# Performance work log

Hardware: AMD Instinct MI355X
Metric: run time of the kernel (lower is better)

The kernel has to match this reference:

```python
import jax, jax.numpy as jnp
import numpy as np
from jax import lax
from jax.scipy.special import logsumexp

B, T, H, K = 64, 512, 1024, 8


def crf_nll(logits, tags, mask, trans):
    """Negative log-likelihood summed over batch (allennlp-style linear-chain CRF,
    no start/end transitions). logits [B,T,K], tags [B,T] int, mask [B,T] float, trans [K,K]."""
    def step(alpha, x):
        logit_t, m_t = x  # [B,K], [B]
        inner = alpha[:, :, None] + trans[None, :, :] + logit_t[:, None, :]  # [B,K,K]
        new = logsumexp(inner, axis=1)
        alpha = jnp.where(m_t[:, None] > 0, new, alpha)
        return alpha, None
    alpha, _ = lax.scan(step, logits[:, 0], (jnp.swapaxes(logits[:, 1:], 0, 1), mask[:, 1:].T))
    logZ = logsumexp(alpha, axis=-1)  # [B]
    emit = jnp.take_along_axis(logits, tags[..., None], axis=-1)[..., 0]  # [B,T]
    emit_score = jnp.sum(emit * mask, axis=-1)
    trans_score = jnp.sum(trans[tags[:, :-1], tags[:, 1:]] * mask[:, 1:], axis=-1)
    return -jnp.sum(emit_score + trans_score - logZ)


def viterbi(logits, trans):
    """Batched Viterbi decode with all-ones mask (as in the original forward).
    logits [B,T,K], trans [K,K] -> tags [B,T] int."""
    def step(alpha, logit_t):
        scores = alpha[:, :, None] + trans[None, :, :]  # [B,K_prev,K_next]
        bp = jnp.argmax(scores, axis=1)                 # [B,K]
        alpha = jnp.max(scores, axis=1) + logit_t
        return alpha, bp
    alpha, bps = lax.scan(step, logits[:, 0], jnp.swapaxes(logits[:, 1:], 0, 1))
    last = jnp.argmax(alpha, axis=-1)  # [B]
    def back(tag, bp):
        prev = jnp.take_along_axis(bp, tag[:, None], axis=1)[:, 0]
        return prev, prev
    _, prevs = lax.scan(back, last, bps, reverse=True)  # [T-1,B]
    return jnp.concatenate([prevs, last[None, :]], axis=0).T  # [B,T]


def setup_inputs():
    key = jax.random.key(0)
    ks = jax.random.split(key, 12)
    encoding = jax.random.normal(ks[0], (B, T, H), dtype=jnp.float32)
    raw = jax.random.randint(ks[1], (B, 3 * T), 0, K).astype(jnp.int32)
    offsets = jnp.concatenate([jnp.zeros(T, jnp.int32), jnp.full((T,), 8, jnp.int32), jnp.full((T,), 16, jnp.int32)])
    labels = raw + offsets[None, :]
    len_tokens = jax.random.randint(ks[2], (B,), 1, T + 1).astype(jnp.int32)
    s = 1.0 / np.sqrt(H)
    W_task = jax.random.uniform(ks[3], (H, K), jnp.float32, -s, s)
    b_task = jax.random.uniform(ks[4], (K,), jnp.float32, -s, s)
    W_process = jax.random.uniform(ks[5], (H, K), jnp.float32, -s, s)
    b_process = jax.random.uniform(ks[6], (K,), jnp.float32, -s, s)
    W_material = jax.random.uniform(ks[7], (H, K), jnp.float32, -s, s)
    b_material = jax.random.uniform(ks[8], (K,), jnp.float32, -s, s)
    trans_task = jax.random.normal(ks[9], (K, K), jnp.float32) * 0.1
    trans_process = jax.random.normal(ks[10], (K, K), jnp.float32) * 0.1
    trans_material = jax.random.normal(ks[11], (K, K), jnp.float32) * 0.1
    return {"encoding": encoding, "labels": labels, "len_tokens": len_tokens,
            "W_task": W_task, "b_task": b_task, "W_process": W_process, "b_process": b_process,
            "W_material": W_material, "b_material": b_material,
            "trans_task": trans_task, "trans_process": trans_process, "trans_material": trans_material}


def reference(encoding, labels, len_tokens, W_task, b_task, W_process, b_process,
              W_material, b_material, trans_task, trans_process, trans_material):
    task_logits = encoding @ W_task + b_task          # [B,T,K]
    process_logits = encoding @ W_process + b_process
    material_logits = encoding @ W_material + b_material
    logits3 = jnp.stack([task_logits, process_logits, material_logits])   # [3,B,T,K]
    trans3 = jnp.stack([trans_task, trans_process, trans_material])       # [3,K,K]
    # Viterbi with all-ones mask, as in the original forward
    tags3 = jax.vmap(viterbi)(logits3, trans3)  # [3,B,T]
    predicted_tags = jnp.concatenate([tags3[0], tags3[1] + 8, tags3[2] + 16], axis=1)  # [B,3T]
    # CRF NLL losses with length mask (training/validation path)
    mask = (jnp.arange(T)[None, :] < len_tokens[:, None]).astype(jnp.float32)
    labels3 = jnp.stack([labels[:, :T], labels[:, T:2 * T] - 8, labels[:, 2 * T:] - 16])
    loss = jnp.sum(jax.vmap(crf_nll, in_axes=(0, 0, None, 0))(logits3, labels3, mask, trans3))
    return task_logits, process_logits, material_logits, predicted_tags, loss
```

## Files before the change

kernel.cpp:

```cpp
#include <hip/hip_runtime.h>
#include <hip/hip_bf16.h>
#include <math.h>

#define BATCH 64
#define TT 512
#define HH 1024
#define KK 8
#define ROWS (BATCH * TT)
#define SEG  (ROWS * KK)
#define TAGS_OFF (3 * SEG)
#define LOSS_OFF (TAGS_OFF + BATCH * 3 * TT)

__global__ __launch_bounds__(256, 2) void gemm_heads(
    const float* __restrict__ enc,
    const float* __restrict__ Wt, const float* __restrict__ bt,
    const float* __restrict__ Wp, const float* __restrict__ bpv,
    const float* __restrict__ Wm, const float* __restrict__ bm,
    float* __restrict__ out)
{
    __shared__ float xt[4][2][16][68];
    __shared__ float wl[4][2][16][32];
    __shared__ float biasl[24];

    int tid  = threadIdx.x;
    int lane = tid & 63;
    int w    = __builtin_amdgcn_readfirstlane(tid >> 6);
    int r    = lane >> 2;
    int q    = lane & 3;
    int rowblk = blockIdx.x * 64;

    if (tid < 24) {
        int hd = tid >> 3, cl = tid & 7;
        biasl[tid] = (hd == 0) ? bt[cl] : (hd == 1) ? bpv[cl] : bm[cl];
    }

    const float* encw = enc + (size_t)rowblk * HH + w * 256;
    const float* Wkt = Wt + w * 2048;
    const float* Wkp = Wp + w * 2048;
    const float* Wkm = Wm + w * 2048;

    int srow = lane >> 2;
    int schunk = lane & 3;

    float acc[24];
#pragma unroll
    for (int c = 0; c < 24; ++c) acc[c] = 0.f;

    float4 sreg[4];
    float  wreg[6];

#define LOADT(it)                                                             \
    {                                                                         \
        _Pragma("unroll")                                                     \
        for (int i = 0; i < 4; ++i)                                           \
            sreg[i] = *(const float4*)(encw + (size_t)(srow + 16 * i) * HH +  \
                                       (it) * 16 + schunk * 4);               \
    }
#define WRITET(buf)                                                           \
    {                                                                         \
        _Pragma("unroll")                                                     \
        for (int i = 0; i < 4; ++i) {                                         \
            xt[w][buf][schunk * 4 + 0][srow + 16 * i] = sreg[i].x;            \
            xt[w][buf][schunk * 4 + 1][srow + 16 * i] = sreg[i].y;            \
            xt[w][buf][schunk * 4 + 2][srow + 16 * i] = sreg[i].z;            \
            xt[w][buf][schunk * 4 + 3][srow + 16 * i] = sreg[i].w;            \
        }                                                                     \
    }
#define WLOADG(it)                                                            \
    {                                                                         \
        wreg[0] = Wkt[(it) * 128 + lane]; wreg[1] = Wkt[(it) * 128 + 64 + lane]; \
        wreg[2] = Wkp[(it) * 128 + lane]; wreg[3] = Wkp[(it) * 128 + 64 + lane]; \
        wreg[4] = Wkm[(it) * 128 + lane]; wreg[5] = Wkm[(it) * 128 + 64 + lane]; \
    }
#define WWRITE(buf)                                                           \
    {                                                                         \
        int col_ = lane & 7;                                                  \
        _Pragma("unroll")                                                     \
        for (int i = 0; i < 6; ++i) {                                         \
            int hh_ = (lane >> 3) + 8 * (i & 1);                              \
            int c_  = 8 * (i >> 1) + col_;                                    \
            int q_  = (c_ * 43) >> 8;                                         \
            int s_  = c_ - 6 * q_;                                            \
            wl[w][buf][hh_][8 * (q_ ^ (hh_ & 3)) + s_] = wreg[i];             \
        }                                                                     \
    }

    LOADT(0)
    WLOADG(0)
    WRITET(0)
    WWRITE(0)

    for (int it = 0; it < 16; ++it) {
        int cb = it & 1;
        if (it < 15) {
            LOADT(it + 1)
            WLOADG(it + 1)
        }
#pragma unroll
        for (int hh = 0; hh < 16; ++hh) {
            float4 xv = *(const float4*)&xt[w][cb][hh][4 * r];
            const float* wp_ = &wl[w][cb][hh][8 * (q ^ (hh & 3))];
            float4 w0 = *(const float4*)wp_;
            float2 w1 = *(const float2*)(wp_ + 4);
#pragma unroll
            for (int j = 0; j < 4; ++j) {
                float xe = (j == 0) ? xv.x : (j == 1) ? xv.y : (j == 2) ? xv.z : xv.w;
                acc[j * 6 + 0] = fmaf(xe, w0.x, acc[j * 6 + 0]);
                acc[j * 6 + 1] = fmaf(xe, w0.y, acc[j * 6 + 1]);
                acc[j * 6 + 2] = fmaf(xe, w0.z, acc[j * 6 + 2]);
                acc[j * 6 + 3] = fmaf(xe, w0.w, acc[j * 6 + 3]);
                acc[j * 6 + 4] = fmaf(xe, w1.x, acc[j * 6 + 4]);
                acc[j * 6 + 5] = fmaf(xe, w1.y, acc[j * 6 + 5]);
            }
        }
        if (it < 15) {
            WRITET(cb ^ 1)
            WWRITE(cb ^ 1)
        }
    }
#undef LOADT
#undef WRITET
#undef WLOADG
#undef WWRITE

    __syncthreads();
    float* xf = &xt[0][0][0][0];
    int myrow = 4 * r;
    if (w != 0) {
        float* sl = xf + w * 1600;
#pragma unroll
        for (int j = 0; j < 4; ++j)
#pragma unroll
            for (int s = 0; s < 6; ++s)
                sl[(myrow + j) * 25 + q * 6 + s] = acc[j * 6 + s];
    }
    __syncthreads();
    if (w == 0) {
#pragma unroll
        for (int j = 0; j < 4; ++j)
#pragma unroll
            for (int s = 0; s < 6; ++s)
                xf[(myrow + j) * 25 + q * 6 + s] =
                    acc[j * 6 + s] + xf[1600 + (myrow + j) * 25 + q * 6 + s]
                                   + xf[3200 + (myrow + j) * 25 + q * 6 + s]
                                   + xf[4800 + (myrow + j) * 25 + q * 6 + s];
    }
    __syncthreads();
#pragma unroll
    for (int i = 0; i < 2; ++i) {
        int flat = tid + 256 * i;
        if (flat < 384) {
            int seg  = flat >> 7;
            int rem  = flat & 127;
            int row  = rem >> 1;
            int half = rem & 1;
            float4 v;
            v.x = xf[row * 25 + seg * 8 + half * 4 + 0] + biasl[seg * 8 + half * 4 + 0];
            v.y = xf[row * 25 + seg * 8 + half * 4 + 1] + biasl[seg * 8 + half * 4 + 1];
            v.z = xf[row * 25 + seg * 8 + half * 4 + 2] + biasl[seg * 8 + half * 4 + 2];
            v.w = xf[row * 25 + seg * 8 + half * 4 + 3] + biasl[seg * 8 + half * 4 + 3];
            *(float4*)(out + (size_t)seg * SEG + (size_t)(rowblk + row) * 8 + half * 4) = v;
        }
    }
}

#define DPPF(x, ctrl) __int_as_float(__builtin_amdgcn_update_dpp(              \
    0, __float_as_int(x), ctrl, 0xF, 0xF, true))

__device__ __forceinline__ float bcast8(float x, int lane) {
    float qv = DPPF(x, 0x00);
    float hv = DPPF(qv, 0x141);
    return (lane & 4) ? hv : qv;
}

#define GATHER8(ao, r0, r1, r2, r3, r4, r5, r6, r7)                            \
    {                                                                          \
        float s1_ = DPPF(ao, 0xB1);                                            \
        float s2_ = DPPF(ao, 0x4E);                                            \
        float s3_ = DPPF(s1_, 0x4E);                                           \
        float s7_ = DPPF(ao, 0x141);                                           \
        float s6_ = DPPF(s1_, 0x141);                                          \
        float s5_ = DPPF(s2_, 0x141);                                          \
        float s4_ = DPPF(s3_, 0x141);                                          \
        r0 = ao; r1 = s1_; r2 = s2_; r3 = s3_;                                 \
        r4 = s7_; r5 = s6_; r6 = s5_; r7 = s4_;                                \
    }

__device__ __forceinline__ float rfl(float x) {
    return __int_as_float(__builtin_amdgcn_readfirstlane(__float_as_int(x)));
}

__global__ __launch_bounds__(128) void crf_vit(
    const float* __restrict__ logits,
    const int* __restrict__ labels,
    const int* __restrict__ lens,
    const float* __restrict__ trans_t,
    const float* __restrict__ trans_p,
    const float* __restrict__ trans_m,
    float* __restrict__ out_tags,
    float* __restrict__ partial)
{
    __shared__ float llds[TT * KK];
    __shared__ __align__(16) float alds[TT * KK];
    __shared__ unsigned bpw[TT * 2];
    __shared__ unsigned fmapw[64][2];
    __shared__ unsigned char bnd[64];

    int blk = blockIdx.x;
    int h   = blk >> 6;
    int b   = blk & 63;
    int tid = threadIdx.x;
    int wid = __builtin_amdgcn_readfirstlane(tid >> 6);
    int lane = tid & 63;
    int p = lane & 7;
    unsigned char* bpb = (unsigned char*)bpw;

    const float* L = logits + ((size_t)h * BATCH + b) * (TT * KK);
    const float4* Lv = (const float4*)L;
    float4* lv = (float4*)llds;
#pragma unroll
    for (int i = 0; i < 8; ++i) lv[tid + 128 * i] = Lv[tid + 128 * i];
    __syncthreads();

    const float* TR = (h == 0) ? trans_t : (h == 1) ? trans_p : trans_m;
    int len = lens[b];

    if (wid == 0) {
        float Tc0 = TR[(p ^ 0) * 8 + p], Tc1 = TR[(p ^ 1) * 8 + p];
        float Tc2 = TR[(p ^ 2) * 8 + p], Tc3 = TR[(p ^ 3) * 8 + p];
        float Tc4 = TR[(p ^ 7) * 8 + p], Tc5 = TR[(p ^ 6) * 8 + p];
        float Tc6 = TR[(p ^ 5) * 8 + p], Tc7 = TR[(p ^ 4) * 8 + p];

        float av = llds[p];
        if (lane < 8) alds[lane] = av;
        float r0, r1, r2, r3, r4, r5, r6, r7;
        GATHER8(av, r0, r1, r2, r3, r4, r5, r6, r7)

#define VSTEP(t, LT)                                                           \
    {                                                                          \
        float m0 = r0 + Tc0, m1 = r1 + Tc1, m2 = r2 + Tc2, m3 = r3 + Tc3;      \
        float m4 = r4 + Tc4, m5 = r5 + Tc5, m6 = r6 + Tc6, m7 = r7 + Tc7;      \
        float x01 = fmaxf(m0, m1), x23 = fmaxf(m2, m3);                        \
        float x45 = fmaxf(m4, m5), x67 = fmaxf(m6, m7);                        \
        av = fmaxf(fmaxf(x01, x23), fmaxf(x45, x67)) + (LT);                   \
        if (lane < 8) alds[(t) * 8 + p] = av;                                  \
        GATHER8(av, r0, r1, r2, r3, r4, r5, r6, r7)                            \
    }

        for (int c = 0; c < 15; ++c) {
            int tb = 1 + 32 * c;
            float lt[32];
#pragma unroll
            for (int j = 0; j < 32; ++j) lt[j] = llds[(tb + j) * 8 + p];
            __builtin_amdgcn_sched_barrier(0);
#pragma unroll
            for (int j = 0; j < 32; ++j) VSTEP(tb + j, lt[j])
        }
        {
            float lt[31];
#pragma unroll
            for (int j = 0; j < 31; ++j) lt[j] = llds[(481 + j) * 8 + p];
            __builtin_amdgcn_sched_barrier(0);
#pragma unroll
            for (int j = 0; j < 31; ++j) VSTEP(481 + j, lt[j])
        }
#undef VSTEP

        asm volatile("" ::: "memory");

        float4 f03 = *(const float4*)&alds[511 * 8];
        float4 f47 = *(const float4*)&alds[511 * 8 + 4];
        float fv = f03.x; int last_ = 0; float nf;
        nf = f03.y; if (nf > fv) { fv = nf; last_ = 1; }
        nf = f03.z; if (nf > fv) { fv = nf; last_ = 2; }
        nf = f03.w; if (nf > fv) { fv = nf; last_ = 3; }
        nf = f47.x; if (nf > fv) { fv = nf; last_ = 4; }
        nf = f47.y; if (nf > fv) { fv = nf; last_ = 5; }
        nf = f47.z; if (nf > fv) { fv = nf; last_ = 6; }
        nf = f47.w; if (nf > fv) { fv = nf; last_ = 7; }

        {
            int c = lane >> 3;
            int kn = lane & 7;
            float T0 = TR[0 * 8 + kn], T1 = TR[1 * 8 + kn];
            float T2 = TR[2 * 8 + kn], T3 = TR[3 * 8 + kn];
            float T4 = TR[4 * 8 + kn], T5 = TR[5 * 8 + kn];
            float T6 = TR[6 * 8 + kn], T7 = TR[7 * 8 + kn];
            for (int j = 0; j < 64; ++j) {
                int t = c * 64 + j + 1;
                if (t <= 511) {
                    float4 a03 = *(const float4*)&alds[(t - 1) * 8];
                    float4 a47 = *(const float4*)&alds[(t - 1) * 8 + 4];
                    float v = a03.x + T0; int vi = 0; float nv;
                    nv = a03.y + T1; if (nv > v) { v = nv; vi = 1; }
                    nv = a03.z + T2; if (nv > v) { v = nv; vi = 2; }
                    nv = a03.w + T3; if (nv > v) { v = nv; vi = 3; }
                    nv = a47.x + T4; if (nv > v) { v = nv; vi = 4; }
                    nv = a47.y + T5; if (nv > v) { v = nv; vi = 5; }
                    nv = a47.z + T6; if (nv > v) { v = nv; vi = 6; }
                    nv = a47.w + T7; if (nv > v) { v = nv; vi = 7; }
                    bpb[t * 8 + kn] = (unsigned char)vi;
                }
            }
        }
        asm volatile("" ::: "memory");

        int t0 = lane * 8;
        unsigned rw[16];
#pragma unroll
        for (int j = 0; j < 8; ++j) {
            int t = t0 + 1 + j;
            if (t <= 511) { rw[2 * j] = bpw[t * 2]; rw[2 * j + 1] = bpw[t * 2 + 1]; }
            else          { rw[2 * j] = 0x03020100u; rw[2 * j + 1] = 0x07060504u; }
        }
        unsigned sv[8];
#pragma unroll
        for (int i = 0; i < 8; ++i) sv[i] = i;
#pragma unroll
        for (int j = 7; j >= 0; --j) {
            unsigned d0 = rw[2 * j], d1 = rw[2 * j + 1];
#pragma unroll
            for (int i = 0; i < 8; ++i) {
                unsigned s = sv[i];
                unsigned d = (s < 4) ? d0 : d1;
                sv[i] = (d >> (8 * (s & 3))) & 0xffu;
            }
        }
        fmapw[lane][0] = sv[0] | (sv[1] << 8) | (sv[2] << 16) | (sv[3] << 24);
        fmapw[lane][1] = sv[4] | (sv[5] << 8) | (sv[6] << 16) | (sv[7] << 24);
        asm volatile("" ::: "memory");

        if (lane == 0) {
            unsigned cur = (unsigned)last_;
            for (int l = 63; l >= 0; --l) {
                unsigned d = (cur < 4) ? fmapw[l][0] : fmapw[l][1];
                cur = (d >> (8 * (cur & 3))) & 0xffu;
                bnd[l] = (unsigned char)cur;
            }
        }
        asm volatile("" ::: "memory");

        int off = h * 8;
        float* otag = out_tags + b * (3 * TT) + h * TT;
        unsigned curr = (lane == 63) ? (unsigned)last_ : (unsigned)bnd[lane + 1];
#pragma unroll
        for (int j = 7; j >= 0; --j) {
            unsigned d = (curr < 4) ? rw[2 * j] : rw[2 * j + 1];
            curr = (d >> (8 * (curr & 3))) & 0xffu;
            otag[t0 + j] = (float)((int)curr + off);
        }
    } else {
        float E0 = __expf(TR[(p ^ 0) * 8 + p]), E1 = __expf(TR[(p ^ 1) * 8 + p]);
        float E2 = __expf(TR[(p ^ 2) * 8 + p]), E3 = __expf(TR[(p ^ 3) * 8 + p]);
        float E4 = __expf(TR[(p ^ 7) * 8 + p]), E5 = __expf(TR[(p ^ 6) * 8 + p]);
        float E6 = __expf(TR[(p ^ 5) * 8 + p]), E7 = __expf(TR[(p ^ 4) * 8 + p]);

        float a0 = llds[p];
        float c0 = bcast8(a0, lane);
        float S  = __expf(a0 - c0);
        float Mc = c0;

#define LSTEP(t, F_, RN)                                                       \
    {                                                                          \
        if (RN) {                                                              \
            float sref = bcast8(S, lane);                                      \
            float gg = __logf(sref);                                           \
            S *= __expf(-gg);                                                  \
            Mc += gg;                                                          \
        }                                                                      \
        float r0, r1, r2, r3, r4, r5, r6, r7;                                  \
        GATHER8(S, r0, r1, r2, r3, r4, r5, r6, r7)                             \
        float p0 = r0 * E0, p1 = r1 * E1, p2 = r2 * E2, p3 = r3 * E3;          \
        float p4 = r4 * E4, p5 = r5 * E5, p6 = r6 * E6, p7 = r7 * E7;          \
        float ss = ((p0 + p1) + (p2 + p3)) + ((p4 + p5) + (p6 + p7));          \
        float Sn = ss * (F_);                                                  \
        S = ((t) < len) ? Sn : S;                                              \
    }

        for (int c = 0; c < 15; ++c) {
            int tb = 1 + 32 * c;
            float F[32];
#pragma unroll
            for (int j = 0; j < 32; ++j) F[j] = llds[(tb + j) * 8 + p];
#pragma unroll
            for (int j = 0; j < 32; ++j) F[j] = __expf(F[j]);
            __builtin_amdgcn_sched_barrier(0);
#pragma unroll
            for (int j = 0; j < 32; ++j) LSTEP(tb + j, F[j], (j & 3) == 0)
        }
        {
            float F[31];
#pragma unroll
            for (int j = 0; j < 31; ++j) F[j] = llds[(481 + j) * 8 + p];
#pragma unroll
            for (int j = 0; j < 31; ++j) F[j] = __expf(F[j]);
            __builtin_amdgcn_sched_barrier(0);
#pragma unroll
            for (int j = 0; j < 31; ++j) LSTEP(481 + j, F[j], (j & 3) == 0)
        }
#undef LSTEP

        float s1 = S + DPPF(S, 0xB1);
        float s2 = s1 + DPPF(s1, 0x4E);
        float sum8 = s2 + DPPF(s2, 0x141);
        float logZ = Mc + __logf(sum8);

        const int* lab = labels + b * (3 * TT) + h * TT;
        int off = h * 8;
        float sc = 0.f;
#pragma unroll
        for (int j = 0; j < 8; ++j) {
            int t = lane + 64 * j;
            if (t < len) {
                int tg = lab[t] - off;
                sc += llds[t * 8 + tg];
                if (t >= 1) {
                    int tp = lab[t - 1] - off;
                    sc += TR[tp * 8 + tg];
                }
            }
        }
#pragma unroll
        for (int d = 1; d <= 32; d <<= 1) sc += __shfl_xor(sc, d);

        if (lane == 0) partial[blk] = logZ - sc;
    }
}

__global__ __launch_bounds__(64) void loss_reduce(
    const float* __restrict__ partial, float* __restrict__ out_loss)
{
    int lane = threadIdx.x;
    float s = partial[lane] + partial[lane + 64] + partial[lane + 128];
#pragma unroll
    for (int d = 1; d <= 32; d <<= 1) s += __shfl_xor(s, d);
    if (lane == 0) *out_loss = s;
}

extern "C" void kernel_launch(void* const* d_in, const int* in_sizes, int n_in,
                              void* d_out, int out_size, void* d_ws, size_t ws_size,
                              hipStream_t stream) {
    const float* enc    = (const float*)d_in[0];
    const int*   labels = (const int*)d_in[1];
    const int*   lens   = (const int*)d_in[2];
    const float* Wt     = (const float*)d_in[3];
    const float* bt     = (const float*)d_in[4];
    const float* Wp     = (const float*)d_in[5];
    const float* bpv    = (const float*)d_in[6];
    const float* Wm     = (const float*)d_in[7];
    const float* bm     = (const float*)d_in[8];
    const float* tr_t   = (const float*)d_in[9];
    const float* tr_p   = (const float*)d_in[10];
    const float* tr_m   = (const float*)d_in[11];

    float* out = (float*)d_out;
    float* lpart = (float*)d_ws;

    gemm_heads<<<ROWS / 64, 256, 0, stream>>>(enc, Wt, bt, Wp, bpv, Wm, bm, out);
    crf_vit<<<192, 128, 0, stream>>>(out, labels, lens, tr_t, tr_p, tr_m,
                                     out + TAGS_OFF, lpart);
    loss_reduce<<<1, 64, 0, stream>>>(lpart, out + LOSS_OFF);
}
```

Before: 70.55 us.

## Merge Viterbi and forward-algorithm waves into one interleaved single-wave CRF kernel

The CRF kernel previously used two waves per block, one computing the Viterbi max recurrence and backtrace and the other the logsumexp partition function. Both recurrences now run in a single 64-thread wave, interleaved per time step so each dependency chain can hide the other's latency. The forward-algorithm renormalization is restructured so its log/exp is applied one group later, off the critical chain. This trades wave-level concurrency for instruction-level parallelism and halves the block size, and it serializes the backtrace and the label score after both recursions.

```diff
diff --git a/kernel.cpp b/kernel.cpp
--- a/kernel.cpp
+++ b/kernel.cpp
@@ -186,11 +186,7 @@
         r4 = s7_; r5 = s6_; r6 = s5_; r7 = s4_;                                \
     }
 
-__device__ __forceinline__ float rfl(float x) {
-    return __int_as_float(__builtin_amdgcn_readfirstlane(__float_as_int(x)));
-}
-
-__global__ __launch_bounds__(128) void crf_vit(
+__global__ __launch_bounds__(64) void crf_vit(
     const float* __restrict__ logits,
     const int* __restrict__ labels,
     const int* __restrict__ lens,
@@ -209,9 +205,7 @@
     int blk = blockIdx.x;
     int h   = blk >> 6;
     int b   = blk & 63;
-    int tid = threadIdx.x;
-    int wid = __builtin_amdgcn_readfirstlane(tid >> 6);
-    int lane = tid & 63;
+    int lane = threadIdx.x;
     int p = lane & 7;
     unsigned char* bpb = (unsigned char*)bpw;
 
@@ -219,154 +213,44 @@
     const float4* Lv = (const float4*)L;
     float4* lv = (float4*)llds;
 #pragma unroll
-    for (int i = 0; i < 8; ++i) lv[tid + 128 * i] = Lv[tid + 128 * i];
+    for (int i = 0; i < 16; ++i) lv[lane + 64 * i] = Lv[lane + 64 * i];
     __syncthreads();
 
     const float* TR = (h == 0) ? trans_t : (h == 1) ? trans_p : trans_m;
     int len = lens[b];
 
-    if (wid == 0) {
-        float Tc0 = TR[(p ^ 0) * 8 + p], Tc1 = TR[(p ^ 1) * 8 + p];
-        float Tc2 = TR[(p ^ 2) * 8 + p], Tc3 = TR[(p ^ 3) * 8 + p];
-        float Tc4 = TR[(p ^ 7) * 8 + p], Tc5 = TR[(p ^ 6) * 8 + p];
-        float Tc6 = TR[(p ^ 5) * 8 + p], Tc7 = TR[(p ^ 4) * 8 + p];
-
-        float av = llds[p];
-        if (lane < 8) alds[lane] = av;
-        float r0, r1, r2, r3, r4, r5, r6, r7;
-        GATHER8(av, r0, r1, r2, r3, r4, r5, r6, r7)
-
-#define VSTEP(t, LT)                                                           \
+    float Tc0 = TR[(p ^ 0) * 8 + p], Tc1 = TR[(p ^ 1) * 8 + p];
+    float Tc2 = TR[(p ^ 2) * 8 + p], Tc3 = TR[(p ^ 3) * 8 + p];
+    float Tc4 = TR[(p ^ 7) * 8 + p], Tc5 = TR[(p ^ 6) * 8 + p];
+    float Tc6 = TR[(p ^ 5) * 8 + p], Tc7 = TR[(p ^ 4) * 8 + p];
+    float E0 = __expf(Tc0), E1 = __expf(Tc1), E2 = __expf(Tc2), E3 = __expf(Tc3);
+    float E4 = __expf(Tc4), E5 = __expf(Tc5), E6 = __expf(Tc6), E7 = __expf(Tc7);
+
+    float av = llds[p];
+    if (lane < 8) alds[lane] = av;
+    float c0 = bcast8(av, lane);
+    float S  = __expf(av - c0);
+    float Mc = c0;
+    float g = 0.f, eg = 1.f;
+
+#define VSTEP(LT, AVH)                                                         \
     {                                                                          \
+        float r0, r1, r2, r3, r4, r5, r6, r7;                                  \
+        GATHER8(av, r0, r1, r2, r3, r4, r5, r6, r7)                            \
         float m0 = r0 + Tc0, m1 = r1 + Tc1, m2 = r2 + Tc2, m3 = r3 + Tc3;      \
         float m4 = r4 + Tc4, m5 = r5 + Tc5, m6 = r6 + Tc6, m7 = r7 + Tc7;      \
         float x01 = fmaxf(m0, m1), x23 = fmaxf(m2, m3);                        \
         float x45 = fmaxf(m4, m5), x67 = fmaxf(m6, m7);                        \
         av = fmaxf(fmaxf(x01, x23), fmaxf(x45, x67)) + (LT);                   \
-        if (lane < 8) alds[(t) * 8 + p] = av;                                  \
-        GATHER8(av, r0, r1, r2, r3, r4, r5, r6, r7)                            \
-    }
-
-        for (int c = 0; c < 15; ++c) {
-            int tb = 1 + 32 * c;
-            float lt[32];
-#pragma unroll
-            for (int j = 0; j < 32; ++j) lt[j] = llds[(tb + j) * 8 + p];
-            __builtin_amdgcn_sched_barrier(0);
-#pragma unroll
-            for (int j = 0; j < 32; ++j) VSTEP(tb + j, lt[j])
-        }
-        {
-            float lt[31];
-#pragma unroll
-            for (int j = 0; j < 31; ++j) lt[j] = llds[(481 + j) * 8 + p];
-            __builtin_amdgcn_sched_barrier(0);
-#pragma unroll
-            for (int j = 0; j < 31; ++j) VSTEP(481 + j, lt[j])
-        }
-#undef VSTEP
-
-        asm volatile("" ::: "memory");
-
-        float4 f03 = *(const float4*)&alds[511 * 8];
-        float4 f47 = *(const float4*)&alds[511 * 8 + 4];
-        float fv = f03.x; int last_ = 0; float nf;
-        nf = f03.y; if (nf > fv) { fv = nf; last_ = 1; }
-        nf = f03.z; if (nf > fv) { fv = nf; last_ = 2; }
-        nf = f03.w; if (nf > fv) { fv = nf; last_ = 3; }
-        nf = f47.x; if (nf > fv) { fv = nf; last_ = 4; }
-        nf = f47.y; if (nf > fv) { fv = nf; last_ = 5; }
-        nf = f47.z; if (nf > fv) { fv = nf; last_ = 6; }
-        nf = f47.w; if (nf > fv) { fv = nf; last_ = 7; }
-
-        {
-            int c = lane >> 3;
-            int kn = lane & 7;
-            float T0 = TR[0 * 8 + kn], T1 = TR[1 * 8 + kn];
-            float T2 = TR[2 * 8 + kn], T3 = TR[3 * 8 + kn];
-            float T4 = TR[4 * 8 + kn], T5 = TR[5 * 8 + kn];
-            float T6 = TR[6 * 8 + kn], T7 = TR[7 * 8 + kn];
-            for (int j = 0; j < 64; ++j) {
-                int t = c * 64 + j + 1;
-                if (t <= 511) {
-                    float4 a03 = *(const float4*)&alds[(t - 1) * 8];
-                    float4 a47 = *(const float4*)&alds[(t - 1) * 8 + 4];
-                    float v = a03.x + T0; int vi = 0; float nv;
-                    nv = a03.y + T1; if (nv > v) { v = nv; vi = 1; }
-                    nv = a03.z + T2; if (nv > v) { v = nv; vi = 2; }
-                    nv = a03.w + T3; if (nv > v) { v = nv; vi = 3; }
-                    nv = a47.x + T4; if (nv > v) { v = nv; vi = 4; }
-                    nv = a47.y + T5; if (nv > v) { v = nv; vi = 5; }
-                    nv = a47.z + T6; if (nv > v) { v = nv; vi = 6; }
-                    nv = a47.w + T7; if (nv > v) { v = nv; vi = 7; }
-                    bpb[t * 8 + kn] = (unsigned char)vi;
-                }
-            }
-        }
-        asm volatile("" ::: "memory");
-
-        int t0 = lane * 8;
-        unsigned rw[16];
-#pragma unroll
-        for (int j = 0; j < 8; ++j) {
-            int t = t0 + 1 + j;
-            if (t <= 511) { rw[2 * j] = bpw[t * 2]; rw[2 * j + 1] = bpw[t * 2 + 1]; }
-            else          { rw[2 * j] = 0x03020100u; rw[2 * j + 1] = 0x07060504u; }
-        }
-        unsigned sv[8];
-#pragma unroll
-        for (int i = 0; i < 8; ++i) sv[i] = i;
-#pragma unroll
-        for (int j = 7; j >= 0; --j) {
-            unsigned d0 = rw[2 * j], d1 = rw[2 * j + 1];
-#pragma unroll
-            for (int i = 0; i < 8; ++i) {
-                unsigned s = sv[i];
-                unsigned d = (s < 4) ? d0 : d1;
-                sv[i] = (d >> (8 * (s & 3))) & 0xffu;
-            }
-        }
-        fmapw[lane][0] = sv[0] | (sv[1] << 8) | (sv[2] << 16) | (sv[3] << 24);
-        fmapw[lane][1] = sv[4] | (sv[5] << 8) | (sv[6] << 16) | (sv[7] << 24);
-        asm volatile("" ::: "memory");
-
-        if (lane == 0) {
-            unsigned cur = (unsigned)last_;
-            for (int l = 63; l >= 0; --l) {
-                unsigned d = (cur < 4) ? fmapw[l][0] : fmapw[l][1];
-                cur = (d >> (8 * (cur & 3))) & 0xffu;
-                bnd[l] = (unsigned char)cur;
-            }
-        }
-        asm volatile("" ::: "memory");
-
-        int off = h * 8;
-        float* otag = out_tags + b * (3 * TT) + h * TT;
-        unsigned curr = (lane == 63) ? (unsigned)last_ : (unsigned)bnd[lane + 1];
-#pragma unroll
-        for (int j = 7; j >= 0; --j) {
-            unsigned d = (curr < 4) ? rw[2 * j] : rw[2 * j + 1];
-            curr = (d >> (8 * (curr & 3))) & 0xffu;
-            otag[t0 + j] = (float)((int)curr + off);
-        }
-    } else {
-        float E0 = __expf(TR[(p ^ 0) * 8 + p]), E1 = __expf(TR[(p ^ 1) * 8 + p]);
-        float E2 = __expf(TR[(p ^ 2) * 8 + p]), E3 = __expf(TR[(p ^ 3) * 8 + p]);
-        float E4 = __expf(TR[(p ^ 7) * 8 + p]), E5 = __expf(TR[(p ^ 6) * 8 + p]);
-        float E6 = __expf(TR[(p ^ 5) * 8 + p]), E7 = __expf(TR[(p ^ 4) * 8 + p]);
-
-        float a0 = llds[p];
-        float c0 = bcast8(a0, lane);
-        float S  = __expf(a0 - c0);
-        float Mc = c0;
-
+        AVH = av;                                                              \
+    }
 #define LSTEP(t, F_, RN)                                                       \
     {                                                                          \
         if (RN) {                                                              \
+            S *= eg; Mc += g;                                                  \
             float sref = bcast8(S, lane);                                      \
-            float gg = __logf(sref);                                           \
-            S *= __expf(-gg);                                                  \
-            Mc += gg;                                                          \
+            g = __logf(sref);                                                  \
+            eg = __expf(-g);                                                   \
         }                                                                      \
         float r0, r1, r2, r3, r4, r5, r6, r7;                                  \
         GATHER8(S, r0, r1, r2, r3, r4, r5, r6, r7)                             \
@@ -377,54 +261,151 @@
         S = ((t) < len) ? Sn : S;                                              \
     }
 
-        for (int c = 0; c < 15; ++c) {
-            int tb = 1 + 32 * c;
-            float F[32];
-#pragma unroll
-            for (int j = 0; j < 32; ++j) F[j] = llds[(tb + j) * 8 + p];
-#pragma unroll
-            for (int j = 0; j < 32; ++j) F[j] = __expf(F[j]);
-            __builtin_amdgcn_sched_barrier(0);
-#pragma unroll
-            for (int j = 0; j < 32; ++j) LSTEP(tb + j, F[j], (j & 3) == 0)
-        }
-        {
-            float F[31];
-#pragma unroll
-            for (int j = 0; j < 31; ++j) F[j] = llds[(481 + j) * 8 + p];
-#pragma unroll
-            for (int j = 0; j < 31; ++j) F[j] = __expf(F[j]);
-            __builtin_amdgcn_sched_barrier(0);
-#pragma unroll
-            for (int j = 0; j < 31; ++j) LSTEP(481 + j, F[j], (j & 3) == 0)
-        }
+    for (int c = 0; c < 15; ++c) {
+        int tb = 1 + 32 * c;
+        float lt[32], F[32], avh[32];
+#pragma unroll
+        for (int j = 0; j < 32; ++j) lt[j] = llds[(tb + j) * 8 + p];
+#pragma unroll
+        for (int j = 0; j < 32; ++j) F[j] = __expf(lt[j]);
+        __builtin_amdgcn_sched_barrier(0);
+#pragma unroll
+        for (int j = 0; j < 32; ++j) {
+            VSTEP(lt[j], avh[j])
+            LSTEP(tb + j, F[j], (j & 3) == 0)
+        }
+        if (lane < 8) {
+#pragma unroll
+            for (int j = 0; j < 32; ++j) alds[(tb + j) * 8 + p] = avh[j];
+        }
+    }
+    {
+        float lt[31], F[31], avh[31];
+#pragma unroll
+        for (int j = 0; j < 31; ++j) lt[j] = llds[(481 + j) * 8 + p];
+#pragma unroll
+        for (int j = 0; j < 31; ++j) F[j] = __expf(lt[j]);
+        __builtin_amdgcn_sched_barrier(0);
+#pragma unroll
+        for (int j = 0; j < 31; ++j) {
+            VSTEP(lt[j], avh[j])
+            LSTEP(481 + j, F[j], (j & 3) == 0)
+        }
+        if (lane < 8) {
+#pragma unroll
+            for (int j = 0; j < 31; ++j) alds[(481 + j) * 8 + p] = avh[j];
+        }
+    }
+#undef VSTEP
 #undef LSTEP
 
-        float s1 = S + DPPF(S, 0xB1);
-        float s2 = s1 + DPPF(s1, 0x4E);
-        float sum8 = s2 + DPPF(s2, 0x141);
-        float logZ = Mc + __logf(sum8);
-
-        const int* lab = labels + b * (3 * TT) + h * TT;
-        int off = h * 8;
-        float sc = 0.f;
-#pragma unroll
-        for (int j = 0; j < 8; ++j) {
-            int t = lane + 64 * j;
-            if (t < len) {
-                int tg = lab[t] - off;
-                sc += llds[t * 8 + tg];
-                if (t >= 1) {
-                    int tp = lab[t - 1] - off;
-                    sc += TR[tp * 8 + tg];
-                }
+    float s1 = S + DPPF(S, 0xB1);
+    float s2 = s1 + DPPF(s1, 0x4E);
+    float sum8 = s2 + DPPF(s2, 0x141);
+    float logZ = Mc + __logf(sum8);
+
+    asm volatile("" ::: "memory");
+
+    float4 f03 = *(const float4*)&alds[511 * 8];
+    float4 f47 = *(const float4*)&alds[511 * 8 + 4];
+    float fv = f03.x; int last_ = 0; float nf;
+    nf = f03.y; if (nf > fv) { fv = nf; last_ = 1; }
+    nf = f03.z; if (nf > fv) { fv = nf; last_ = 2; }
+    nf = f03.w; if (nf > fv) { fv = nf; last_ = 3; }
+    nf = f47.x; if (nf > fv) { fv = nf; last_ = 4; }
+    nf = f47.y; if (nf > fv) { fv = nf; last_ = 5; }
+    nf = f47.z; if (nf > fv) { fv = nf; last_ = 6; }
+    nf = f47.w; if (nf > fv) { fv = nf; last_ = 7; }
+
+    {
+        int c = lane >> 3;
+        int kn = lane & 7;
+        float T0 = TR[0 * 8 + kn], T1 = TR[1 * 8 + kn];
+        float T2 = TR[2 * 8 + kn], T3 = TR[3 * 8 + kn];
+        float T4 = TR[4 * 8 + kn], T5 = TR[5 * 8 + kn];
+        float T6 = TR[6 * 8 + kn], T7 = TR[7 * 8 + kn];
+        for (int j = 0; j < 64; ++j) {
+            int t = c * 64 + j + 1;
+            if (t <= 511) {
+                float4 a03 = *(const float4*)&alds[(t - 1) * 8];
+                float4 a47 = *(const float4*)&alds[(t - 1) * 8 + 4];
+                float v = a03.x + T0; int vi = 0; float nv;
+                nv = a03.y + T1; if (nv > v) { v = nv; vi = 1; }
+                nv = a03.z + T2; if (nv > v) { v = nv; vi = 2; }
+                nv = a03.w + T3; if (nv > v) { v = nv; vi = 3; }
+                nv = a47.x + T4; if (nv > v) { v = nv; vi = 4; }
+                nv = a47.y + T5; if (nv > v) { v = nv; vi = 5; }
+                nv = a47.z + T6; if (nv > v) { v = nv; vi = 6; }
+                nv = a47.w + T7; if (nv > v) { v = nv; vi = 7; }
+                bpb[t * 8 + kn] = (unsigned char)vi;
             }
         }
-#pragma unroll
-        for (int d = 1; d <= 32; d <<= 1) sc += __shfl_xor(sc, d);
-
-        if (lane == 0) partial[blk] = logZ - sc;
-    }
+    }
+    asm volatile("" ::: "memory");
+
+    int t0 = lane * 8;
+    unsigned rw[16];
+#pragma unroll
+    for (int j = 0; j < 8; ++j) {
+        int t = t0 + 1 + j;
+        if (t <= 511) { rw[2 * j] = bpw[t * 2]; rw[2 * j + 1] = bpw[t * 2 + 1]; }
+        else          { rw[2 * j] = 0x03020100u; rw[2 * j + 1] = 0x07060504u; }
+    }
+    unsigned sv[8];
+#pragma unroll
+    for (int i = 0; i < 8; ++i) sv[i] = i;
+#pragma unroll
+    for (int j = 7; j >= 0; --j) {
+        unsigned d0 = rw[2 * j], d1 = rw[2 * j + 1];
+#pragma unroll
+        for (int i = 0; i < 8; ++i) {
+            unsigned s = sv[i];
+            unsigned d = (s < 4) ? d0 : d1;
+            sv[i] = (d >> (8 * (s & 3))) & 0xffu;
+        }
+    }
+    fmapw[lane][0] = sv[0] | (sv[1] << 8) | (sv[2] << 16) | (sv[3] << 24);
+    fmapw[lane][1] = sv[4] | (sv[5] << 8) | (sv[6] << 16) | (sv[7] << 24);
+    asm volatile("" ::: "memory");
+
+    if (lane == 0) {
+        unsigned cur = (unsigned)last_;
+        for (int l = 63; l >= 0; --l) {
+            unsigned d = (cur < 4) ? fmapw[l][0] : fmapw[l][1];
+            cur = (d >> (8 * (cur & 3))) & 0xffu;
+            bnd[l] = (unsigned char)cur;
+        }
+    }
+    asm volatile("" ::: "memory");
+
+    int off = h * 8;
+    float* otag = out_tags + b * (3 * TT) + h * TT;
+    unsigned curr = (lane == 63) ? (unsigned)last_ : (unsigned)bnd[lane + 1];
+#pragma unroll
+    for (int j = 7; j >= 0; --j) {
+        unsigned d = (curr < 4) ? rw[2 * j] : rw[2 * j + 1];
+        curr = (d >> (8 * (curr & 3))) & 0xffu;
+        otag[t0 + j] = (float)((int)curr + off);
+    }
+
+    const int* lab = labels + b * (3 * TT) + h * TT;
+    float sc = 0.f;
+#pragma unroll
+    for (int j = 0; j < 8; ++j) {
+        int t = lane + 64 * j;
+        if (t < len) {
+            int tg = lab[t] - off;
+            sc += llds[t * 8 + tg];
+            if (t >= 1) {
+                int tp = lab[t - 1] - off;
+                sc += TR[tp * 8 + tg];
+            }
+        }
+    }
+#pragma unroll
+    for (int d = 1; d <= 32; d <<= 1) sc += __shfl_xor(sc, d);
+
+    if (lane == 0) partial[blk] = logZ - sc;
 }
 
 __global__ __launch_bounds__(64) void loss_reduce(
@@ -457,7 +438,7 @@
     float* lpart = (float*)d_ws;
 
     gemm_heads<<<ROWS / 64, 256, 0, stream>>>(enc, Wt, bt, Wp, bpv, Wm, bm, out);
-    crf_vit<<<192, 128, 0, stream>>>(out, labels, lens, tr_t, tr_p, tr_m,
-                                     out + TAGS_OFF, lpart);
+    crf_vit<<<192, 64, 0, stream>>>(out, labels, lens, tr_t, tr_p, tr_m,
+                                    out + TAGS_OFF, lpart);
     loss_reduce<<<1, 64, 0, stream>>>(lpart, out + LOSS_OFF);
 }
```

Result: slower. 94.40 us (+33.8%).
